# Kernel tuning notes

Measured on AMD Instinct MI355X. Metric: run time of the kernel, lower is better.

The kernel has to match this reference:

```python
import jax, jax.numpy as jnp
import numpy as np

EPS_NORM = 1e-12  # torch F.normalize eps
EPS_SQRT = 1e-6
EPS_DIV = 1e-6


def setup_inputs() -> dict:
    key = jax.random.key(0)
    k1, k2, k3 = jax.random.split(key, 3)
    B, K, D, C = 4096, 32768, 256, 100
    def l2n(x):
        return x / jnp.maximum(jnp.linalg.norm(x, axis=1, keepdims=True), EPS_NORM)
    batch_feature = l2n(jax.random.normal(k1, (B, D), dtype=jnp.float32))
    queue_emb_copy = l2n(jax.random.normal(k2, (K, D), dtype=jnp.float32))
    info_label = jax.random.randint(k3, (K,), 0, C, dtype=jnp.int64 if jax.config.jax_enable_x64 else jnp.int32)
    return {"batch_feature": batch_feature, "queue_emb_copy": queue_emb_copy,
            "info_label": info_label, "num_classes": C}


def reference(batch_feature, queue_emb_copy, info_label, num_classes):
    # Per-class centroids: segment-mean over the queue (replaces the torch.where loop).
    counts = jax.ops.segment_sum(jnp.ones((queue_emb_copy.shape[0],), queue_emb_copy.dtype),
                                 info_label, num_segments=num_classes)  # [C]
    sums = jax.ops.segment_sum(queue_emb_copy, info_label, num_segments=num_classes)  # [C, D]
    centroids = sums / counts[:, None]
    centroids_norm = centroids / jnp.maximum(jnp.linalg.norm(centroids, axis=1, keepdims=True), EPS_NORM)

    # Pseudo-labels from similarity to centroids.
    similarity_matrix_cls = batch_feature @ centroids_norm.T  # [B, C]
    pseudo_label = jnp.argmax(similarity_matrix_cls, axis=1)  # [B]
    mask = (pseudo_label[:, None] == info_label[None, :])     # [B, K] bool

    # Pairwise MAE distances (unit-norm embeddings: MSE = 2 - 2*cos).
    sim_matrix = jnp.einsum('bc,kc->bk', batch_feature, jax.lax.stop_gradient(queue_emb_copy))
    MAE_matrix = jnp.sqrt(2.0 - 2.0 * sim_matrix + EPS_SQRT)  # [B, K]

    maskf = mask.astype(MAE_matrix.dtype)
    min_entropy_loss = jnp.mean(jnp.sum(MAE_matrix * maskf, axis=1) / (jnp.sum(maskf, axis=1) + EPS_DIV))
    maskc = 1.0 - maskf
    avg_inter_cluster_dist = jnp.mean(jnp.sum(MAE_matrix * maskc, axis=1) / (jnp.sum(maskc, axis=1) + EPS_DIV))
    max_entropy_loss = 2.0 - avg_inter_cluster_dist
    return min_entropy_loss + max_entropy_loss
```

## Files before the change

kernel.cpp:

```cpp
#include <hip/hip_runtime.h>

#define B_ROWS 4096
#define K_Q    32768
#define D_DIM  256
#define C_CLS  100

typedef unsigned char u8;
typedef long i64;
typedef __attribute__((ext_vector_type(2))) long i64x2;
typedef __attribute__((ext_vector_type(4))) float f32x4;

__device__ inline float fast_sqrt(float x) { return __builtin_amdgcn_sqrtf(x); }

#define GLDS16(g, l) __builtin_amdgcn_global_load_lds( \
    (const __attribute__((address_space(1))) unsigned int*)(g), \
    (__attribute__((address_space(3))) unsigned int*)(l), 16, 0, 0)


__global__ __launch_bounds__(512) void k_hist(
    const float* __restrict__ q, const int* __restrict__ lab,
    float* __restrict__ partial, u8* __restrict__ qf8,
    float* __restrict__ S_all, float* __restrict__ S_match) {
  __shared__ float lsum[C_CLS * 64];
  const int kc = blockIdx.x, dc = blockIdx.y;
  const int tid = threadIdx.x, w = tid >> 6, l = tid & 63;
  if (dc == 0 && tid < 64) {
    S_all[kc * 64 + tid] = 0.f;
    S_match[kc * 64 + tid] = 0.f;
  }
  for (int i = tid; i < C_CLS * 64; i += 512) lsum[i] = 0.f;
  __syncthreads();
  const int col = dc * 64 + l;
  const int pcol = ((l >> 3) & 3) * 64 + (dc * 2 + (l >> 5)) * 8 + (l & 7);
  const int k0 = kc * 512 + w * 64;
  #pragma unroll 4
  for (int r = 0; r < 64; ++r) {
    const int k = k0 + r;
    const int c = lab[k];
    float v = q[(size_t)k * D_DIM + col];
    atomicAdd(&lsum[c * 64 + l], v);
    int p8 = __builtin_amdgcn_cvt_pk_fp8_f32(v * 16.f, v * 16.f, 0, false);
    qf8[(size_t)k * D_DIM + pcol] = (u8)p8;
  }
  __syncthreads();
  float* pb = partial + (size_t)(kc * 4 + dc) * (C_CLS * 64);
  for (int i = tid; i < C_CLS * 64; i += 512) pb[i] = lsum[i];
}

__global__ __launch_bounds__(256) void k_cnorm(
    const int* __restrict__ lab, const float* __restrict__ partial,
    int* __restrict__ counts, float* __restrict__ cnorm) {
  __shared__ float red[4];
  __shared__ int credi[4];
  const int c = blockIdx.x, d = threadIdx.x;
  int cnt = 0;
  #pragma unroll 8
  for (int i = 0; i < K_Q / 256; ++i) cnt += (lab[d + i * 256] == c) ? 1 : 0;
  #pragma unroll
  for (int o = 1; o < 64; o <<= 1) cnt += __shfl_xor(cnt, o);
  if ((d & 63) == 0) credi[d >> 6] = cnt;
  float s = 0.f;
  const int dcsel = d >> 6, low = d & 63;
  for (int kc = 0; kc < 64; ++kc)
    s += partial[(size_t)(kc * 4 + dcsel) * (C_CLS * 64) + c * 64 + low];
  __syncthreads();
  const int cnt_all = credi[0] + credi[1] + credi[2] + credi[3];
  float v = s / (float)cnt_all;
  float ss = v * v;
  #pragma unroll
  for (int o = 1; o < 64; o <<= 1) ss += __shfl_xor(ss, o);
  if ((d & 63) == 0) red[d >> 6] = ss;
  __syncthreads();
  float norm = sqrtf(red[0] + red[1] + red[2] + red[3]);
  cnorm[c * D_DIM + d] = v / fmaxf(norm, 1e-12f);
  if (d == 0) counts[c] = cnt_all;
}

__global__ void k_pseudo(const float* __restrict__ bf, const float* __restrict__ cn,
                         int* __restrict__ pseudo, u8* __restrict__ af8) {
  const int tid = threadIdx.x;
  const int rloc = tid >> 4, sub = tid & 15;
  const int row = blockIdx.x * 16 + rloc;
  float4 a[4];
  const float4* ap = (const float4*)(bf + (size_t)row * D_DIM);
  #pragma unroll
  for (int j = 0; j < 4; ++j) a[j] = ap[sub + j * 16];
  const int hi_ = (sub >> 1) & 3, b0_ = 4 * (sub & 1), ktb = sub >> 3;
  #pragma unroll
  for (int j = 0; j < 4; ++j) {
    int lo = __builtin_amdgcn_cvt_pk_fp8_f32(a[j].x * 16.f, a[j].y * 16.f, 0, false);
    int pk = __builtin_amdgcn_cvt_pk_fp8_f32(a[j].z * 16.f, a[j].w * 16.f, lo, true);
    const int kt = 2 * j + ktb;
    *(unsigned int*)(af8 + (size_t)row * D_DIM + hi_ * 64 + kt * 8 + b0_) = (unsigned int)pk;
  }
  float best = -1e30f; int bi = 0;
  for (int c = 0; c < C_CLS; c += 2) {
    const float4* cp0 = (const float4*)(cn + c * D_DIM);
    const float4* cp1 = (const float4*)(cn + (c + 1) * D_DIM);
    float s0 = 0.f, s1 = 0.f;
    #pragma unroll
    for (int j = 0; j < 4; ++j) {
      float4 b0 = cp0[sub + j * 16];
      float4 b1 = cp1[sub + j * 16];
      s0 += a[j].x * b0.x + a[j].y * b0.y + a[j].z * b0.z + a[j].w * b0.w;
      s1 += a[j].x * b1.x + a[j].y * b1.y + a[j].z * b1.z + a[j].w * b1.w;
    }
    s0 += __shfl_xor(s0, 1); s1 += __shfl_xor(s1, 1);
    s0 += __shfl_xor(s0, 2); s1 += __shfl_xor(s1, 2);
    s0 += __shfl_xor(s0, 4); s1 += __shfl_xor(s1, 4);
    s0 += __shfl_xor(s0, 8); s1 += __shfl_xor(s1, 8);
    if (s0 > best) { best = s0; bi = c; }
    if (s1 > best) { best = s1; bi = c + 1; }
  }
  if (sub == 0) pseudo[row] = bi;
}

__global__ __launch_bounds__(512, 4) void k_main(
    const u8* __restrict__ Af8, const u8* __restrict__ Qf8,
    const int* __restrict__ lab, const int* __restrict__ pseudo,
    float* __restrict__ S_all, float* __restrict__ S_match) {
  __shared__ u8 Bs[2][64 * 256];

  const int bid = blockIdx.x;
  const int xcd = bid & 7, idx = bid >> 3;
  const int cs = xcd * 4 + (idx >> 4);
  const int rb = idx & 15;

  const int tid = threadIdx.x;
  const int w = tid >> 6, l = tid & 63;
  const int q16 = l & 15, hi = l >> 4;
  const int rowA = rb * 256 + w * 32;
  const int colbase = cs * 1024;

  i64x2 areg[2][4];
  #pragma unroll
  for (int m = 0; m < 2; ++m) {
    const u8* ap = Af8 + (size_t)(rowA + m * 16 + q16) * D_DIM + hi * 64;
    #pragma unroll
    for (int kt2 = 0; kt2 < 4; ++kt2)
      areg[m][kt2] = *(const i64x2*)(ap + kt2 * 16);
  }

  int psepk[2];
  #pragma unroll
  for (int m = 0; m < 2; ++m) {
    const int* pp = pseudo + rowA + m * 16 + hi * 4;
    psepk[m] = pp[0] | (pp[1] << 8) | (pp[2] << 16) | (pp[3] << 24);
  }

  float pa[2][4], pm_[2][4];
  #pragma unroll
  for (int m = 0; m < 2; ++m)
    #pragma unroll
    for (int j = 0; j < 4; ++j) { pa[m][j] = 0.f; pm_[m][j] = 0.f; }

  const int scol = tid >> 4;
  const int sinner = ((tid & 15) * 16) ^ ((scol & 7) << 4);
  const u8* sbase = Qf8 + (size_t)(colbase + scol) * D_DIM + sinner;

#define STAGE(buf, ph)                                                    \
  { const u8* s_ = sbase + (size_t)(ph) * (64 * D_DIM);                   \
    GLDS16(s_,                 (buf) + tid * 16);                         \
    GLDS16(s_ + 32 * D_DIM,    (buf) + 8192 + tid * 16); }

  const int* lptr = lab + colbase + q16;
  const int xorm = (q16 & 7) << 4;
  const f32x4 fzero = {0.f, 0.f, 0.f, 0.f};

  STAGE(&Bs[0][0], 0);

  #pragma unroll 1
  for (int ph = 0; ph < 16; ++ph) {
    __syncthreads();
    if (ph + 1 < 16) STAGE(&Bs[(ph + 1) & 1][0], ph + 1);
    const u8* bs = &Bs[ph & 1][0];
    int lbl[4];
    #pragma unroll
    for (int n = 0; n < 4; ++n) lbl[n] = lptr[ph * 64 + n * 16];

    f32x4 acc[2][4];
    #pragma unroll
    for (int kt2 = 0; kt2 < 4; ++kt2) {
      const int koff = (hi * 64 + kt2 * 16) ^ xorm;
      i64x2 b[4];
      #pragma unroll
      for (int n = 0; n < 4; ++n)
        b[n] = *(const i64x2*)(bs + (n * 16 + q16) * 256 + koff);
      #pragma unroll
      for (int m = 0; m < 2; ++m)
        #pragma unroll
        for (int n = 0; n < 4; ++n) {
          acc[m][n] = __builtin_amdgcn_mfma_f32_16x16x32_fp8_fp8(
              areg[m][kt2].x, b[n].x, kt2 == 0 ? fzero : acc[m][n], 0, 0, 0);
          acc[m][n] = __builtin_amdgcn_mfma_f32_16x16x32_fp8_fp8(
              areg[m][kt2].y, b[n].y, acc[m][n], 0, 0, 0);
        }
    }

    #pragma unroll
    for (int m = 0; m < 2; ++m)
      #pragma unroll
      for (int j = 0; j < 4; ++j) {
        const int p = (psepk[m] >> (8 * j)) & 255;
        #pragma unroll
        for (int n = 0; n < 4; ++n) {
          float mae = fast_sqrt(fmaxf(__builtin_fmaf(-0.0078125f, acc[m][n][j], 2.000001f), 0.0f));
          pa[m][j] += mae;
          pm_[m][j] += (lbl[n] == p ? mae : 0.0f);
        }
      }
  }

  #pragma unroll
  for (int m = 0; m < 2; ++m)
    #pragma unroll
    for (int j = 0; j < 4; ++j) {
      float va = pa[m][j], vm = pm_[m][j];
      va += __shfl_xor(va, 1); va += __shfl_xor(va, 2);
      va += __shfl_xor(va, 4); va += __shfl_xor(va, 8);
      vm += __shfl_xor(vm, 1); vm += __shfl_xor(vm, 2);
      vm += __shfl_xor(vm, 4); vm += __shfl_xor(vm, 8);
      if (q16 == 0) {
        const int gr = rowA + m * 16 + hi * 4 + j;
        atomicAdd(&S_all[gr], va);
        atomicAdd(&S_match[gr], vm);
      }
    }
#undef STAGE
}

__global__ void k_final(const float* __restrict__ S_all, const float* __restrict__ S_match,
                        const int* __restrict__ pseudo, const int* __restrict__ counts,
                        float* __restrict__ out) {
  __shared__ float r1[16], r2[16];
  const int tid = threadIdx.x;
  float s1 = 0.f, s2 = 0.f;
  for (int b = tid; b < B_ROWS; b += 1024) {
    float cnt = (float)counts[pseudo[b]];
    float sm = S_match[b], sa = S_all[b];
    s1 += sm / (cnt + 1e-6f);
    s2 += (sa - sm) / ((float)K_Q - cnt + 1e-6f);
  }
  #pragma unroll
  for (int o = 1; o < 64; o <<= 1) { s1 += __shfl_xor(s1, o); s2 += __shfl_xor(s2, o); }
  if ((tid & 63) == 0) { r1[tid >> 6] = s1; r2[tid >> 6] = s2; }
  __syncthreads();
  if (tid == 0) {
    float t1 = 0.f, t2 = 0.f;
    #pragma unroll
    for (int i = 0; i < 16; ++i) { t1 += r1[i]; t2 += r2[i]; }
    out[0] = t1 / (float)B_ROWS + 2.0f - t2 / (float)B_ROWS;
  }
}

extern "C" void kernel_launch(void* const* d_in, const int* in_sizes, int n_in,
                              void* d_out, int out_size, void* d_ws, size_t ws_size,
                              hipStream_t stream) {
  const float* batch = (const float*)d_in[0];
  const float* queue = (const float*)d_in[1];
  const int*   lab   = (const int*)d_in[2];

  char* ws = (char*)d_ws;
  float* S_all   = (float*)(ws + 0);
  float* S_match = (float*)(ws + 16384);
  int*   counts  = (int*)  (ws + 32768);
  float* cnorm   = (float*)(ws + 33280);
  int*   pseudo  = (int*)  (ws + 135680);
  u8*    Af8     = (u8*)   (ws + 152064);
  u8*    Qf8     = (u8*)   (ws + 1200640);
  float* partial = (float*)(ws + 9589248);

  k_hist  <<<dim3(64, 4), 512, 0, stream>>>(queue, lab, partial, Qf8, S_all, S_match);
  k_cnorm <<<C_CLS, 256, 0, stream>>>(lab, partial, counts, cnorm);
  k_pseudo<<<B_ROWS / 16, 256, 0, stream>>>(batch, cnorm, pseudo, Af8);
  k_main  <<<512, 512, 0, stream>>>(Af8, Qf8, lab, pseudo, S_all, S_match);
  k_final <<<1, 1024, 0, stream>>>(S_all, S_match, pseudo, counts, (float*)d_out);
}
```

Before: 155.9 us.

## Switch main GEMM to 32x32x64 scaled FP8 MFMA with natural operand layout

Replaces the 16x16x32 fp8 MFMA tiling in the main distance kernel with the gfx950 32x32x64 f8f6f4 scaled MFMA, using unit scales. The A and Q fp8 buffers are now written in natural row-major order instead of the permuted layout. The LDS swizzle changes to a 16-way XOR to suit the new 32-byte operand reads, and the epilogue reduction is adapted to the 32x32 accumulator layout. The aim is fewer MFMA issues and fewer LDS reads per tile, at the cost of larger accumulator register use and some risk of LDS bank conflicts under the new access pattern.

New measurement: 205.3 us. +31.7%, slower.

```diff
diff --git a/kernel.cpp b/kernel.cpp
--- a/kernel.cpp
+++ b/kernel.cpp
@@ -6,11 +6,15 @@
 #define C_CLS  100
 
 typedef unsigned char u8;
-typedef long i64;
-typedef __attribute__((ext_vector_type(2))) long i64x2;
-typedef __attribute__((ext_vector_type(4))) float f32x4;
+typedef __attribute__((ext_vector_type(4))) int i32x4;
+typedef __attribute__((ext_vector_type(8))) int i32x8;
+typedef __attribute__((ext_vector_type(16))) float f32x16;
 
 __device__ inline float fast_sqrt(float x) { return __builtin_amdgcn_sqrtf(x); }
+
+__device__ inline i32x8 mk8(i32x4 lo, i32x4 hi) {
+  return __builtin_shufflevector(lo, hi, 0, 1, 2, 3, 4, 5, 6, 7);
+}
 
 #define GLDS16(g, l) __builtin_amdgcn_global_load_lds( \
     (const __attribute__((address_space(1))) unsigned int*)(g), \
@@ -31,7 +35,6 @@
   for (int i = tid; i < C_CLS * 64; i += 512) lsum[i] = 0.f;
   __syncthreads();
   const int col = dc * 64 + l;
-  const int pcol = ((l >> 3) & 3) * 64 + (dc * 2 + (l >> 5)) * 8 + (l & 7);
   const int k0 = kc * 512 + w * 64;
   #pragma unroll 4
   for (int r = 0; r < 64; ++r) {
@@ -40,7 +43,7 @@
     float v = q[(size_t)k * D_DIM + col];
     atomicAdd(&lsum[c * 64 + l], v);
     int p8 = __builtin_amdgcn_cvt_pk_fp8_f32(v * 16.f, v * 16.f, 0, false);
-    qf8[(size_t)k * D_DIM + pcol] = (u8)p8;
+    qf8[(size_t)k * D_DIM + col] = (u8)p8;
   }
   __syncthreads();
   float* pb = partial + (size_t)(kc * 4 + dc) * (C_CLS * 64);
@@ -85,13 +88,11 @@
   const float4* ap = (const float4*)(bf + (size_t)row * D_DIM);
   #pragma unroll
   for (int j = 0; j < 4; ++j) a[j] = ap[sub + j * 16];
-  const int hi_ = (sub >> 1) & 3, b0_ = 4 * (sub & 1), ktb = sub >> 3;
   #pragma unroll
   for (int j = 0; j < 4; ++j) {
     int lo = __builtin_amdgcn_cvt_pk_fp8_f32(a[j].x * 16.f, a[j].y * 16.f, 0, false);
     int pk = __builtin_amdgcn_cvt_pk_fp8_f32(a[j].z * 16.f, a[j].w * 16.f, lo, true);
-    const int kt = 2 * j + ktb;
-    *(unsigned int*)(af8 + (size_t)row * D_DIM + hi_ * 64 + kt * 8 + b0_) = (unsigned int)pk;
+    *(unsigned int*)(af8 + (size_t)row * D_DIM + (sub + j * 16) * 4) = (unsigned int)pk;
   }
   float best = -1e30f; int bi = 0;
   for (int c = 0; c < C_CLS; c += 2) {
@@ -128,44 +129,43 @@
 
   const int tid = threadIdx.x;
   const int w = tid >> 6, l = tid & 63;
-  const int q16 = l & 15, hi = l >> 4;
+  const int c32 = l & 31, hi32 = l >> 5;
   const int rowA = rb * 256 + w * 32;
   const int colbase = cs * 1024;
 
-  i64x2 areg[2][4];
-  #pragma unroll
-  for (int m = 0; m < 2; ++m) {
-    const u8* ap = Af8 + (size_t)(rowA + m * 16 + q16) * D_DIM + hi * 64;
-    #pragma unroll
-    for (int kt2 = 0; kt2 < 4; ++kt2)
-      areg[m][kt2] = *(const i64x2*)(ap + kt2 * 16);
-  }
-
-  int psepk[2];
-  #pragma unroll
-  for (int m = 0; m < 2; ++m) {
-    const int* pp = pseudo + rowA + m * 16 + hi * 4;
-    psepk[m] = pp[0] | (pp[1] << 8) | (pp[2] << 16) | (pp[3] << 24);
-  }
-
-  float pa[2][4], pm_[2][4];
-  #pragma unroll
-  for (int m = 0; m < 2; ++m)
-    #pragma unroll
-    for (int j = 0; j < 4; ++j) { pa[m][j] = 0.f; pm_[m][j] = 0.f; }
-
-  const int scol = tid >> 4;
-  const int sinner = ((tid & 15) * 16) ^ ((scol & 7) << 4);
-  const u8* sbase = Qf8 + (size_t)(colbase + scol) * D_DIM + sinner;
+  i32x4 areg[4][2];
+  {
+    const u8* ap = Af8 + (size_t)(rowA + c32) * D_DIM + hi32 * 32;
+    #pragma unroll
+    for (int ks = 0; ks < 4; ++ks) {
+      areg[ks][0] = *(const i32x4*)(ap + ks * 64);
+      areg[ks][1] = *(const i32x4*)(ap + ks * 64 + 16);
+    }
+  }
+
+  int psepk[4];
+  #pragma unroll
+  for (int g = 0; g < 4; ++g) {
+    const int* pp = pseudo + rowA + hi32 * 4 + g * 8;
+    psepk[g] = pp[0] | (pp[1] << 8) | (pp[2] << 16) | (pp[3] << 24);
+  }
+
+  float pa[16], pm[16];
+  #pragma unroll
+  for (int r = 0; r < 16; ++r) { pa[r] = 0.f; pm[r] = 0.f; }
+
+  const int strow = tid >> 4;
+  const int sinner = (((tid & 15) ^ (strow & 15)) << 4);
+  const u8* sbase = Qf8 + (size_t)(colbase + strow) * D_DIM + sinner;
 
 #define STAGE(buf, ph)                                                    \
   { const u8* s_ = sbase + (size_t)(ph) * (64 * D_DIM);                   \
-    GLDS16(s_,                 (buf) + tid * 16);                         \
-    GLDS16(s_ + 32 * D_DIM,    (buf) + 8192 + tid * 16); }
-
-  const int* lptr = lab + colbase + q16;
-  const int xorm = (q16 & 7) << 4;
-  const f32x4 fzero = {0.f, 0.f, 0.f, 0.f};
+    GLDS16(s_,              (buf) + tid * 16);                            \
+    GLDS16(s_ + 32 * D_DIM, (buf) + 8192 + tid * 16); }
+
+  const int* lptr = lab + colbase + c32;
+  const int xorm = (c32 & 15) << 4;
+  const unsigned int SC1 = 0x7F7F7F7Fu;
 
   STAGE(&Bs[0][0], 0);
 
@@ -174,58 +174,48 @@
     __syncthreads();
     if (ph + 1 < 16) STAGE(&Bs[(ph + 1) & 1][0], ph + 1);
     const u8* bs = &Bs[ph & 1][0];
-    int lbl[4];
-    #pragma unroll
-    for (int n = 0; n < 4; ++n) lbl[n] = lptr[ph * 64 + n * 16];
-
-    f32x4 acc[2][4];
-    #pragma unroll
-    for (int kt2 = 0; kt2 < 4; ++kt2) {
-      const int koff = (hi * 64 + kt2 * 16) ^ xorm;
-      i64x2 b[4];
-      #pragma unroll
-      for (int n = 0; n < 4; ++n)
-        b[n] = *(const i64x2*)(bs + (n * 16 + q16) * 256 + koff);
-      #pragma unroll
-      for (int m = 0; m < 2; ++m)
-        #pragma unroll
-        for (int n = 0; n < 4; ++n) {
-          acc[m][n] = __builtin_amdgcn_mfma_f32_16x16x32_fp8_fp8(
-              areg[m][kt2].x, b[n].x, kt2 == 0 ? fzero : acc[m][n], 0, 0, 0);
-          acc[m][n] = __builtin_amdgcn_mfma_f32_16x16x32_fp8_fp8(
-              areg[m][kt2].y, b[n].y, acc[m][n], 0, 0, 0);
-        }
-    }
-
-    #pragma unroll
-    for (int m = 0; m < 2; ++m)
-      #pragma unroll
-      for (int j = 0; j < 4; ++j) {
-        const int p = (psepk[m] >> (8 * j)) & 255;
-        #pragma unroll
-        for (int n = 0; n < 4; ++n) {
-          float mae = fast_sqrt(fmaxf(__builtin_fmaf(-0.0078125f, acc[m][n][j], 2.000001f), 0.0f));
-          pa[m][j] += mae;
-          pm_[m][j] += (lbl[n] == p ? mae : 0.0f);
-        }
-      }
-  }
-
-  #pragma unroll
-  for (int m = 0; m < 2; ++m)
-    #pragma unroll
-    for (int j = 0; j < 4; ++j) {
-      float va = pa[m][j], vm = pm_[m][j];
-      va += __shfl_xor(va, 1); va += __shfl_xor(va, 2);
-      va += __shfl_xor(va, 4); va += __shfl_xor(va, 8);
-      vm += __shfl_xor(vm, 1); vm += __shfl_xor(vm, 2);
-      vm += __shfl_xor(vm, 4); vm += __shfl_xor(vm, 8);
-      if (q16 == 0) {
-        const int gr = rowA + m * 16 + hi * 4 + j;
-        atomicAdd(&S_all[gr], va);
-        atomicAdd(&S_match[gr], vm);
-      }
-    }
+    const int lbl0 = lptr[ph * 64];
+    const int lbl1 = lptr[ph * 64 + 32];
+
+    f32x16 acc0{}, acc1{};
+    #pragma unroll
+    for (int ks = 0; ks < 4; ++ks) {
+      const int off = ks * 64 + hi32 * 32;
+      i32x4 b0l = *(const i32x4*)(bs + c32 * 256 + (off ^ xorm));
+      i32x4 b0h = *(const i32x4*)(bs + c32 * 256 + ((off + 16) ^ xorm));
+      i32x4 b1l = *(const i32x4*)(bs + (32 + c32) * 256 + (off ^ xorm));
+      i32x4 b1h = *(const i32x4*)(bs + (32 + c32) * 256 + ((off + 16) ^ xorm));
+      i32x8 av = mk8(areg[ks][0], areg[ks][1]);
+      acc0 = __builtin_amdgcn_mfma_scale_f32_32x32x64_f8f6f4(
+          av, mk8(b0l, b0h), acc0, 0, 0, 0, SC1, 0, SC1);
+      acc1 = __builtin_amdgcn_mfma_scale_f32_32x32x64_f8f6f4(
+          av, mk8(b1l, b1h), acc1, 0, 0, 0, SC1, 0, SC1);
+    }
+
+    #pragma unroll
+    for (int r = 0; r < 16; ++r) {
+      const int p = (psepk[r >> 2] >> ((r & 3) * 8)) & 255;
+      float mae0 = fast_sqrt(fmaxf(__builtin_fmaf(-0.0078125f, acc0[r], 2.000001f), 0.0f));
+      float mae1 = fast_sqrt(fmaxf(__builtin_fmaf(-0.0078125f, acc1[r], 2.000001f), 0.0f));
+      pa[r] += mae0 + mae1;
+      pm[r] += (lbl0 == p ? mae0 : 0.0f) + (lbl1 == p ? mae1 : 0.0f);
+    }
+  }
+
+  #pragma unroll
+  for (int r = 0; r < 16; ++r) {
+    float va = pa[r], vm = pm[r];
+    va += __shfl_xor(va, 1); vm += __shfl_xor(vm, 1);
+    va += __shfl_xor(va, 2); vm += __shfl_xor(vm, 2);
+    va += __shfl_xor(va, 4); vm += __shfl_xor(vm, 4);
+    va += __shfl_xor(va, 8); vm += __shfl_xor(vm, 8);
+    va += __shfl_xor(va, 16); vm += __shfl_xor(vm, 16);
+    if (c32 == 0) {
+      const int gr = rowA + (r & 3) + 8 * (r >> 2) + 4 * hi32;
+      atomicAdd(&S_all[gr], va);
+      atomicAdd(&S_match[gr], vm);
+    }
+  }
 #undef STAGE
 }
 
```
